# Kernel optimization log

Hardware: AMD Instinct MI355X
Metric: run time of the kernel (lower is better)

Reference implementation:

```python
import jax, jax.numpy as jnp
import numpy as np

B = 1048576
S = 8
K = 10  # n_facts
EPS = 1e-8
ENTROPY_W = 0.01
DIVERSITY_W = 0.1


def setup_inputs() -> dict:
    key = jax.random.key(0)
    k1, k2, k3, k4, k5 = jax.random.split(key, 5)
    p = jax.random.uniform(k1, (B, 2, K), dtype=jnp.float32) + 1e-3
    pCS = p / jnp.sum(p, axis=-1, keepdims=True)  # normalized probs like Categorical
    base_loss = jax.random.uniform(k2, (1,), dtype=jnp.float32)
    Y = jax.random.randint(k3, (B,), 0, 19, dtype=jnp.int32)
    samples1 = jax.random.randint(k4, (S, B), 0, K, dtype=jnp.int32)
    samples2 = jax.random.randint(k5, (S, B), 0, K, dtype=jnp.int32)
    return {"pCS": pCS, "base_loss": base_loss, "Y": Y,
            "samples1": samples1, "samples2": samples2}


def reference(pCS, base_loss, Y, samples1, samples2):
    n_facts = pCS.shape[-1]
    s = samples1.shape[0]
    p1 = pCS[:, 0, :]  # [B, K]
    p2 = pCS[:, 1, :]
    # entropy regularization
    ent1 = -jnp.sum(p1 * jnp.log(p1 + EPS), axis=-1).mean()
    ent2 = -jnp.sum(p2 * jnp.log(p2 + EPS), axis=-1).mean()
    entropy_loss = -(ent1 + ent2) / 2
    # diversity: count unique (d1,d2) pairs per batch element (vectorized bincount-style)
    pairs = (samples1 * n_facts + samples2).T  # [B, S]
    eq = pairs[:, :, None] == pairs[:, None, :]  # [B, S, S]
    earlier = jnp.tril(jnp.ones((s, s), dtype=bool), k=-1)  # j < i
    dup = jnp.any(eq & earlier[None], axis=-1)  # [B, S] True if seen before
    unique_counts = jnp.sum(~dup, axis=-1).astype(jnp.float32)  # [B]
    diversity = unique_counts.mean()
    max_diversity = min(s, n_facts * n_facts)
    diversity_ratio = diversity / max_diversity
    diversity_loss = -jnp.log(diversity_ratio + EPS)
    # REINFORCE leave-one-out (computed, not added to total in original)
    pred_labels = samples1 + samples2  # [S, B] (addition task)
    correct = (pred_labels == Y[None, :]).astype(jnp.float32)
    sample_acc = correct.mean()
    b_idx = jnp.arange(p1.shape[0])[None, :]
    log_probs = jnp.log(p1)[b_idx, samples1] + jnp.log(p2)[b_idx, samples2]  # [S, B]
    baseline = (jnp.sum(correct, axis=0, keepdims=True) - correct) / (s - 1 + EPS)
    advantage = jax.lax.stop_gradient(correct - baseline)
    rloo_loss = -jnp.mean(log_probs * advantage)
    total_loss = base_loss[0] + ENTROPY_W * entropy_loss + DIVERSITY_W * diversity_loss
    return jnp.stack([total_loss, rloo_loss, diversity_loss, sample_acc])
```

## Files before the change

kernel.cpp:

```cpp
#include <hip/hip_runtime.h>

#define S_CONST 8
#define K_CONST 10
#define EPSF 1e-8f
#define ROWS_PER_TILE 256
#define ROW_PAD 21

__global__ __launch_bounds__(256) void fml_reduce(
        const float* __restrict__ pCS,
        const int* __restrict__ Y,
        const int* __restrict__ s1g,
        const int* __restrict__ s2g,
        double* __restrict__ partials,
        int B)
{
    __shared__ float sp[ROWS_PER_TILE * ROW_PAD];
    __shared__ float red[4][4];

    float ent = 0.f, uniq = 0.f, corr = 0.f, rloo = 0.f;

    const int tid = threadIdx.x;
    const int ntiles = (B + ROWS_PER_TILE - 1) / ROWS_PER_TILE;

    for (int tile = blockIdx.x; tile < ntiles; tile += gridDim.x) {
        const int base = tile * ROWS_PER_TILE;

        const float4* src = reinterpret_cast<const float4*>(pCS + (size_t)base * 20);
        #pragma unroll
        for (int k = 0; k < 5; ++k) {
            int g = tid + (k << 8);
            int r = g / 5;
            int j = g - r * 5;
            float4 v = make_float4(0.f, 0.f, 0.f, 0.f);
            if (base + r < B) v = src[g];
            float* dst = &sp[r * ROW_PAD + j * 4];
            dst[0] = v.x; dst[1] = v.y; dst[2] = v.z; dst[3] = v.w;
        }
        __syncthreads();

        const int row = base + tid;
        if (row < B) {
            const float* my = &sp[tid * ROW_PAD];
            float p1[K_CONST], p2[K_CONST], lg1[K_CONST], lg2[K_CONST];
            #pragma unroll
            for (int j = 0; j < K_CONST; ++j) { p1[j] = my[j]; p2[j] = my[10 + j]; }
            #pragma unroll
            for (int j = 0; j < K_CONST; ++j) {
                lg1[j] = logf(p1[j]);
                lg2[j] = logf(p2[j]);
                ent += p1[j] * lg1[j] + p2[j] * lg2[j];
            }

            const int y = Y[row];

            int a1[S_CONST], a2[S_CONST], pr[S_CONST];
            float c[S_CONST];
            float csum = 0.f;
            #pragma unroll
            for (int s = 0; s < S_CONST; ++s) {
                a1[s] = s1g[(size_t)s * B + row];
                a2[s] = s2g[(size_t)s * B + row];
                pr[s] = a1[s] * K_CONST + a2[s];
                c[s]  = (a1[s] + a2[s] == y) ? 1.f : 0.f;
                csum += c[s];
            }
            corr += csum;

            #pragma unroll
            for (int i = 0; i < S_CONST; ++i) {
                bool dup = false;
                #pragma unroll
                for (int j = 0; j < i; ++j) dup = dup || (pr[i] == pr[j]);
                uniq += dup ? 0.f : 1.f;
            }

            #pragma unroll
            for (int s = 0; s < S_CONST; ++s) {
                float adv = c[s] - (csum - c[s]) / 7.0f;
                float g1 = lg1[0], g2 = lg2[0];
                #pragma unroll
                for (int j = 1; j < K_CONST; ++j) {
                    g1 = (a1[s] == j) ? lg1[j] : g1;
                    g2 = (a2[s] == j) ? lg2[j] : g2;
                }
                rloo += (g1 + g2) * adv;
            }
        }
        __syncthreads();
    }

    #pragma unroll
    for (int off = 32; off >= 1; off >>= 1) {
        ent  += __shfl_xor(ent,  off);
        uniq += __shfl_xor(uniq, off);
        corr += __shfl_xor(corr, off);
        rloo += __shfl_xor(rloo, off);
    }

    const int lane = threadIdx.x & 63;
    const int wave = threadIdx.x >> 6;
    if (lane == 0) {
        red[wave][0] = ent; red[wave][1] = uniq;
        red[wave][2] = corr; red[wave][3] = rloo;
    }
    __syncthreads();
    if (threadIdx.x == 0) {
        double e = 0, u = 0, cs = 0, rl = 0;
        #pragma unroll
        for (int w = 0; w < 4; ++w) {
            e += (double)red[w][0]; u += (double)red[w][1];
            cs += (double)red[w][2]; rl += (double)red[w][3];
        }
        double* p = &partials[(size_t)blockIdx.x * 4];
        p[0] = e; p[1] = u; p[2] = cs; p[3] = rl;
    }
}

__global__ __launch_bounds__(1024) void fml_finalize(
        const double* __restrict__ partials,
        const float* __restrict__ base_loss,
        float* __restrict__ out, int B, int nblocks)
{
    __shared__ double red[16][4];
    double e = 0, u = 0, cs = 0, rl = 0;
    for (int i = threadIdx.x; i < nblocks; i += 1024) {
        const double* p = &partials[(size_t)i * 4];
        e += p[0]; u += p[1]; cs += p[2]; rl += p[3];
    }
    #pragma unroll
    for (int off = 32; off >= 1; off >>= 1) {
        e  += __shfl_xor(e,  off);
        u  += __shfl_xor(u,  off);
        cs += __shfl_xor(cs, off);
        rl += __shfl_xor(rl, off);
    }
    const int lane = threadIdx.x & 63;
    const int wave = threadIdx.x >> 6;
    if (lane == 0) { red[wave][0] = e; red[wave][1] = u; red[wave][2] = cs; red[wave][3] = rl; }
    __syncthreads();
    if (threadIdx.x == 0) {
        e = 0; u = 0; cs = 0; rl = 0;
        #pragma unroll
        for (int w = 0; w < 16; ++w) {
            e += red[w][0]; u += red[w][1]; cs += red[w][2]; rl += red[w][3];
        }
        double dB = (double)B;
        float entropy_loss = (float)(e / (2.0 * dB));
        float diversity = (float)(u / dB);
        float ratio = diversity / 8.0f;
        float diversity_loss = -logf(ratio + EPSF);
        float sample_acc = (float)(cs / (dB * (double)S_CONST));
        float rloo_loss  = (float)(-rl / (dB * (double)S_CONST));
        out[0] = base_loss[0] + 0.01f * entropy_loss + 0.1f * diversity_loss;
        out[1] = rloo_loss;
        out[2] = diversity_loss;
        out[3] = sample_acc;
    }
}

extern "C" void kernel_launch(void* const* d_in, const int* in_sizes, int n_in,
                              void* d_out, int out_size, void* d_ws, size_t ws_size,
                              hipStream_t stream) {
    const float* pCS       = (const float*)d_in[0];
    const float* base_loss = (const float*)d_in[1];
    const int*   Y         = (const int*)d_in[2];
    const int*   s1        = (const int*)d_in[3];
    const int*   s2        = (const int*)d_in[4];
    float* out = (float*)d_out;
    const int B = in_sizes[2];

    double* partials = (double*)d_ws;

    const int block = 256;
    const int grid = 2048;
    fml_reduce<<<grid, block, 0, stream>>>(pCS, Y, s1, s2, partials, B);
    fml_finalize<<<1, 1024, 0, stream>>>(partials, base_loss, out, B, grid);
}
```

Measured before the change: 44.50 us.

## Compute entropy during tile load and gather sampled log-probs from LDS

Entropy terms are now computed directly on each float4 as it is loaded, using fast __logf. The padded per-row scatter into shared memory becomes an unpadded float4 store. The rloo term no longer precomputes 20 logs per row with select chains; it indexes the sampled probabilities from shared memory and takes one __logf of their product per sample, cutting transcendental work and register pressure. This trades the select chains for dynamically indexed LDS reads that may hit bank conflicts (row stride 20), and __logf plus log-of-product reduces accuracy slightly.

```diff
diff --git a/kernel.cpp b/kernel.cpp
--- a/kernel.cpp
+++ b/kernel.cpp
@@ -3,8 +3,7 @@
 #define S_CONST 8
 #define K_CONST 10
 #define EPSF 1e-8f
-#define ROWS_PER_TILE 256
-#define ROW_PAD 21
+#define ROWS 256
 
 __global__ __launch_bounds__(256) void fml_reduce(
         const float* __restrict__ pCS,
@@ -14,43 +13,32 @@
         double* __restrict__ partials,
         int B)
 {
-    __shared__ float sp[ROWS_PER_TILE * ROW_PAD];
+    __shared__ float sp[ROWS * 20];
     __shared__ float red[4][4];
 
     float ent = 0.f, uniq = 0.f, corr = 0.f, rloo = 0.f;
-
     const int tid = threadIdx.x;
-    const int ntiles = (B + ROWS_PER_TILE - 1) / ROWS_PER_TILE;
+    const int ntiles = (B + ROWS - 1) / ROWS;
 
     for (int tile = blockIdx.x; tile < ntiles; tile += gridDim.x) {
-        const int base = tile * ROWS_PER_TILE;
+        const int base = tile * ROWS;
 
         const float4* src = reinterpret_cast<const float4*>(pCS + (size_t)base * 20);
+        float4* dst = reinterpret_cast<float4*>(sp);
+        const bool full = (base + ROWS) <= B;
         #pragma unroll
         for (int k = 0; k < 5; ++k) {
-            int g = tid + (k << 8);
-            int r = g / 5;
-            int j = g - r * 5;
-            float4 v = make_float4(0.f, 0.f, 0.f, 0.f);
-            if (base + r < B) v = src[g];
-            float* dst = &sp[r * ROW_PAD + j * 4];
-            dst[0] = v.x; dst[1] = v.y; dst[2] = v.z; dst[3] = v.w;
+            const int g = tid + (k << 8);
+            float4 v = make_float4(1.f, 1.f, 1.f, 1.f);
+            if (full || (base + g / 5) < B) v = src[g];
+            ent += v.x * __logf(v.x) + v.y * __logf(v.y)
+                 + v.z * __logf(v.z) + v.w * __logf(v.w);
+            dst[g] = v;
         }
         __syncthreads();
 
         const int row = base + tid;
         if (row < B) {
-            const float* my = &sp[tid * ROW_PAD];
-            float p1[K_CONST], p2[K_CONST], lg1[K_CONST], lg2[K_CONST];
-            #pragma unroll
-            for (int j = 0; j < K_CONST; ++j) { p1[j] = my[j]; p2[j] = my[10 + j]; }
-            #pragma unroll
-            for (int j = 0; j < K_CONST; ++j) {
-                lg1[j] = logf(p1[j]);
-                lg2[j] = logf(p2[j]);
-                ent += p1[j] * lg1[j] + p2[j] * lg2[j];
-            }
-
             const int y = Y[row];
 
             int a1[S_CONST], a2[S_CONST], pr[S_CONST];
@@ -74,16 +62,13 @@
                 uniq += dup ? 0.f : 1.f;
             }
 
+            const float* my = &sp[tid * 20];
             #pragma unroll
             for (int s = 0; s < S_CONST; ++s) {
-                float adv = c[s] - (csum - c[s]) / 7.0f;
-                float g1 = lg1[0], g2 = lg2[0];
-                #pragma unroll
-                for (int j = 1; j < K_CONST; ++j) {
-                    g1 = (a1[s] == j) ? lg1[j] : g1;
-                    g2 = (a2[s] == j) ? lg2[j] : g2;
-                }
-                rloo += (g1 + g2) * adv;
+                const float g1 = my[a1[s]];
+                const float g2 = my[10 + a2[s]];
+                const float adv = c[s] - (csum - c[s]) / 7.0f;
+                rloo += __logf(g1 * g2) * adv;
             }
         }
         __syncthreads();
@@ -144,13 +129,13 @@
         for (int w = 0; w < 16; ++w) {
             e += red[w][0]; u += red[w][1]; cs += red[w][2]; rl += red[w][3];
         }
-        double dB = (double)B;
-        float entropy_loss = (float)(e / (2.0 * dB));
-        float diversity = (float)(u / dB);
-        float ratio = diversity / 8.0f;
-        float diversity_loss = -logf(ratio + EPSF);
-        float sample_acc = (float)(cs / (dB * (double)S_CONST));
-        float rloo_loss  = (float)(-rl / (dB * (double)S_CONST));
+        const double dB = (double)B;
+        const float entropy_loss = (float)(e / (2.0 * dB));
+        const float diversity = (float)(u / dB);
+        const float ratio = diversity / 8.0f;
+        const float diversity_loss = -logf(ratio + EPSF);
+        const float sample_acc = (float)(cs / (dB * (double)S_CONST));
+        const float rloo_loss  = (float)(-rl / (dB * (double)S_CONST));
         out[0] = base_loss[0] + 0.01f * entropy_loss + 0.1f * diversity_loss;
         out[1] = rloo_loss;
         out[2] = diversity_loss;
```

After: 42.72 us. 4.0% less time.
